# Kernel optimization log

Hardware: AMD Instinct MI355X
Metric: run time of the kernel (lower is better)

The kernel has to match this reference:

```python
import jax, jax.numpy as jnp
import numpy as np

EPS = 1e-8
TAU = 0.2  # gumbel temperature


def lorentz_linear(x, W, log_scale):
    # y = W x; project back onto hyperboloid (k=1): time from sigmoid, rescale space
    y = x @ W.T
    time = jax.nn.sigmoid(y[..., :1]) * jnp.exp(log_scale) + 1.1
    narrow = y[..., 1:]
    s = (time * time - 1.0) / jnp.clip(jnp.sum(narrow * narrow, axis=-1, keepdims=True), EPS, None)
    return jnp.concatenate([time, narrow * jnp.sqrt(s)], axis=-1)


def logmap0(x):
    # Lorentz (k=1) log map at origin o=(1,0,...,0): (0, arccosh(x0) * xs/||xs||)
    x0 = x[..., :1]
    xs = x[..., 1:]
    nrm = jnp.clip(jnp.linalg.norm(xs, axis=-1, keepdims=True), EPS, None)
    d = jnp.arccosh(jnp.clip(x0, 1.0 + 1e-6, None))
    return jnp.concatenate([jnp.zeros_like(x0), d * xs / nrm], axis=-1)


def lorentz_dist(a, b):
    # dist = arccosh(-<a,b>_L), <a,b>_L = -a0*b0 + sum_i ai*bi
    inner = a[..., 0] * b[..., 0] - jnp.sum(a[..., 1:] * b[..., 1:], axis=-1)
    return jnp.arccosh(jnp.clip(inner, 1.0 + 1e-6, None))


def scatter_softmax(score, seg, num_segments):
    m = jax.ops.segment_max(score, seg, num_segments=num_segments)
    m = jnp.where(jnp.isfinite(m), m, 0.0)  # empty segments
    e = jnp.exp(score - m[seg])
    s = jax.ops.segment_sum(e, seg, num_segments=num_segments)
    return e / jnp.clip(s[seg], EPS, None)


def setup_inputs() -> dict:
    key = jax.random.key(0)
    ks = jax.random.split(key, 8)
    N, E, D, A = 50000, 800000, 128, 128
    # nodes on hyperboloid: time = sqrt(1 + ||space||^2)
    xs = jax.random.normal(ks[0], (N, D - 1), dtype=jnp.float32)
    x0 = jnp.sqrt(1.0 + jnp.sum(xs * xs, axis=-1, keepdims=True))
    x = jnp.concatenate([x0, xs], axis=-1)
    src = jax.random.randint(ks[1], (E,), 0, N)
    dst = jax.random.randint(ks[2], (E,), 0, N)
    edge_value = jax.random.uniform(ks[3], (E,), dtype=jnp.float32)
    stdv = 1.0 / np.sqrt(D)
    Wq = jax.random.uniform(ks[4], (D, D), minval=-stdv, maxval=stdv, dtype=jnp.float32).at[:, 0].set(0.0)
    Wk = jax.random.uniform(ks[5], (D, D), minval=-stdv, maxval=stdv, dtype=jnp.float32).at[:, 0].set(0.0)
    Wa = jax.random.normal(ks[6], (A, D), dtype=jnp.float32) * np.sqrt(2.0 / (A + D))
    log_scale = jnp.asarray(np.log(10.0), dtype=jnp.float32)
    return {"x": x, "src": src, "dst": dst, "edge_value": edge_value,
            "Wq": Wq, "Wk": Wk, "Wa": Wa,
            "log_scale_q": log_scale, "log_scale_k": log_scale}


def reference(x, src, dst, edge_value, Wq, Wk, Wa, log_scale_q, log_scale_k):
    N = x.shape[0]
    # assignment logits in tangent space -> softmax
    ass = jax.nn.softmax(logmap0(x) @ Wa.T, axis=-1)  # [N, A]
    q = lorentz_linear(x, Wq, log_scale_q)            # [N, D]
    k = lorentz_linear(x, Wk, log_scale_k)
    # per-edge negative Lorentz distance
    score = -lorentz_dist(q[src], k[dst])             # [E]
    # scatter softmax over outgoing edges of each src node
    score = scatter_softmax(score, src, N)
    # sparse attention matmul: out[i] = sum_{e: src=i} score_e * ass[dst_e]
    ass = jax.ops.segment_sum(score[:, None] * ass[dst], src, num_segments=N)  # [N, A]
    # gumbel softmax on log(ass + 1e-6)
    logits = jnp.log(ass + 1e-6)
    u = jax.random.uniform(jax.random.key(42), logits.shape, minval=1e-10, maxval=1.0)
    g = -jnp.log(-jnp.log(u))
    return jax.nn.softmax((logits + g) / TAU, axis=-1)
```

## Files before the change

### kernel.cpp

```cpp
#include <hip/hip_runtime.h>
#include <hip/hip_bf16.h>
#include <hip/hip_fp16.h>
#include <math.h>


#define D128 128
#define XP 136

typedef _Float16 f16x2 __attribute__((ext_vector_type(2)));
typedef _Float16 f16x8 __attribute__((ext_vector_type(8)));
typedef float f32x4 __attribute__((ext_vector_type(4)));

union U4 { uint4 u; f16x2 f2[4]; __half2 hh[4]; };

__device__ __forceinline__ void threefry2x32(unsigned x0, unsigned x1,
                                             unsigned& o0, unsigned& o1) {
  const unsigned k0 = 0u, k1 = 42u;
  const unsigned k2 = 0x1BD11BDAu ^ k0 ^ k1;
  x0 += k0; x1 += k1;
#define TF_ROT(r) { x0 += x1; x1 = (x1 << (r)) | (x1 >> (32 - (r))); x1 ^= x0; }
  TF_ROT(13) TF_ROT(15) TF_ROT(26) TF_ROT(6)
  x0 += k1; x1 += k2 + 1u;
  TF_ROT(17) TF_ROT(29) TF_ROT(16) TF_ROT(24)
  x0 += k2; x1 += k0 + 2u;
  TF_ROT(13) TF_ROT(15) TF_ROT(26) TF_ROT(6)
  x0 += k0; x1 += k1 + 3u;
  TF_ROT(17) TF_ROT(29) TF_ROT(16) TF_ROT(24)
  x0 += k1; x1 += k2 + 4u;
  TF_ROT(13) TF_ROT(15) TF_ROT(26) TF_ROT(6)
  x0 += k2; x1 += k0 + 5u;
#undef TF_ROT
  o0 = x0; o1 = x1;
}

__global__ __launch_bounds__(256) void cvt_kernel(
    const float* __restrict__ x, const float* __restrict__ Wq,
    const float* __restrict__ Wk, const float* __restrict__ Wa,
    __half* __restrict__ xh, __half* __restrict__ wqh,
    __half* __restrict__ wkh, __half* __restrict__ wah, int nx8) {
  int i = blockIdx.x * 256 + threadIdx.x;
  const float* src; __half* dst; size_t off;
  if (i < nx8) {
    src = x; dst = xh; off = (size_t)i * 8;
  } else {
    int j = i - nx8; int w = j >> 11; int r = j & 2047;
    if (w >= 3) return;
    off = (size_t)r * 8;
    src = (w == 0) ? Wq : (w == 1) ? Wk : Wa;
    dst = (w == 0) ? wqh : (w == 1) ? wkh : wah;
  }
  float4 a = *reinterpret_cast<const float4*>(src + off);
  float4 b = *reinterpret_cast<const float4*>(src + off + 4);
  union { __half2 h2[4]; uint4 u; } pk;
  pk.h2[0] = __floats2half2_rn(a.x, a.y);
  pk.h2[1] = __floats2half2_rn(a.z, a.w);
  pk.h2[2] = __floats2half2_rn(b.x, b.y);
  pk.h2[3] = __floats2half2_rn(b.z, b.w);
  *reinterpret_cast<uint4*>(dst + off) = pk.u;
}

__global__ __launch_bounds__(256) void gemm_ass_kernel(
    const __half* __restrict__ xh_g, const __half* __restrict__ wh_g,
    __half* __restrict__ out, int N) {
  __shared__ __align__(16) _Float16 xs[64 * XP];
  __shared__ __align__(16) _Float16 wh[128 * XP];

  const int t = threadIdx.x;
  const int row0 = blockIdx.x * 64;

#pragma unroll
  for (int rr = 0; rr < 2; ++rr) {
    int r = (t >> 3) + 32 * rr, tr = t & 7;
    int gr = row0 + r;
    U4 c0, c1;
    c0.u = make_uint4(0, 0, 0, 0); c1.u = make_uint4(0, 0, 0, 0);
    if (gr < N) {
      c0.u = *reinterpret_cast<const uint4*>(xh_g + (size_t)gr * D128 + tr * 16);
      c1.u = *reinterpret_cast<const uint4*>(xh_g + (size_t)gr * D128 + tr * 16 + 8);
    }
    float v[16];
    float ss = 0.f;
#pragma unroll
    for (int j = 0; j < 4; ++j) {
      float2 f = __half22float2(c0.hh[j]);
      v[2 * j] = f.x; v[2 * j + 1] = f.y; ss += f.x * f.x + f.y * f.y;
    }
#pragma unroll
    for (int j = 0; j < 4; ++j) {
      float2 f = __half22float2(c1.hh[j]);
      v[8 + 2 * j] = f.x; v[9 + 2 * j] = f.y; ss += f.x * f.x + f.y * f.y;
    }
    if (tr == 0) ss -= v[0] * v[0];
#pragma unroll
    for (int msk = 1; msk < 8; msk <<= 1) ss += __shfl_xor(ss, msk);
    float x0v = __shfl(v[0], (t & 63) & ~7);
    float dd = acoshf(fmaxf(x0v, 1.f + 1e-6f));
    float sc = dd / fmaxf(sqrtf(ss), 1e-8f);
#pragma unroll
    for (int j = 0; j < 16; ++j) v[j] *= sc;
    if (tr == 0) v[0] = 0.f;
    union { __half2 h2[4]; uint4 u; } pk;
#pragma unroll
    for (int j = 0; j < 4; ++j) pk.h2[j] = __floats2half2_rn(v[2 * j], v[2 * j + 1]);
    *reinterpret_cast<uint4*>(&xs[r * XP + tr * 16]) = pk.u;
#pragma unroll
    for (int j = 0; j < 4; ++j) pk.h2[j] = __floats2half2_rn(v[8 + 2 * j], v[9 + 2 * j]);
    *reinterpret_cast<uint4*>(&xs[r * XP + tr * 16 + 8]) = pk.u;
  }

#pragma unroll
  for (int i = 0; i < 8; ++i) {
    int f = t + 256 * i, wr = f >> 4, c8 = f & 15;
    *reinterpret_cast<uint4*>(&wh[wr * XP + c8 * 8]) =
        *reinterpret_cast<const uint4*>(wh_g + (size_t)wr * D128 + c8 * 8);
  }
  __syncthreads();

  const int w = t >> 6, lane = t & 63;
  const int lc = lane & 15;
  const int arow = 16 * w + lc;
  const int koff = (lane >> 4) * 8;
  f32x4 acc[8];
#pragma unroll
  for (int i = 0; i < 8; ++i) acc[i] = (f32x4){0.f, 0.f, 0.f, 0.f};

#pragma unroll
  for (int kk = 0; kk < 4; ++kk) {
    f16x8 a = *reinterpret_cast<f16x8*>(&xs[arow * XP + kk * 32 + koff]);
#pragma unroll
    for (int tt = 0; tt < 8; ++tt) {
      f16x8 b = *reinterpret_cast<f16x8*>(&wh[(tt * 16 + lc) * XP + kk * 32 + koff]);
      acc[tt] = __builtin_amdgcn_mfma_f32_16x16x32_f16(a, b, acc[tt], 0, 0, 0);
    }
  }

#pragma unroll
  for (int j = 0; j < 4; ++j) {
    int gr = row0 + 16 * w + ((lane >> 4) << 2) + j;
    float mx = acc[0][j];
#pragma unroll
    for (int tt = 1; tt < 8; ++tt) mx = fmaxf(mx, acc[tt][j]);
#pragma unroll
    for (int msk = 1; msk < 16; msk <<= 1) mx = fmaxf(mx, __shfl_xor(mx, msk));
    float e[8], sm = 0.f;
#pragma unroll
    for (int tt = 0; tt < 8; ++tt) { e[tt] = expf(acc[tt][j] - mx); sm += e[tt]; }
#pragma unroll
    for (int msk = 1; msk < 16; msk <<= 1) sm += __shfl_xor(sm, msk);
    float inv = 1.f / sm;
    if (gr < N) {
#pragma unroll
      for (int tt = 0; tt < 8; ++tt)
        out[(size_t)gr * D128 + tt * 16 + lc] = __float2half(e[tt] * inv);
    }
  }
}

__global__ __launch_bounds__(256) void gemm_qk_kernel(
    const __half* __restrict__ xh_g, const __half* __restrict__ wqh_g,
    const __half* __restrict__ wkh_g, const float* __restrict__ lsq,
    const float* __restrict__ lsk, __half* __restrict__ qout,
    __half* __restrict__ kout, int N) {
  __shared__ __align__(16) _Float16 xs[64 * XP];
  __shared__ __align__(16) _Float16 wh[128 * XP];

  const int t = threadIdx.x;
  const int row0 = blockIdx.x * 64;

#pragma unroll
  for (int i = 0; i < 4; ++i) {
    int f = t + 256 * i, r = f >> 4, c8 = f & 15;
    uint4 v = make_uint4(0, 0, 0, 0);
    if (row0 + r < N)
      v = *reinterpret_cast<const uint4*>(xh_g + (size_t)(row0 + r) * D128 + c8 * 8);
    *reinterpret_cast<uint4*>(&xs[r * XP + c8 * 8]) = v;
  }

  const int w = t >> 6, lane = t & 63;
  const int lc = lane & 15;
  const int arow = 16 * w + lc;
  const int koff = (lane >> 4) * 8;

  for (int p = 0; p < 2; ++p) {
    const __half* Wg = p ? wkh_g : wqh_g;
    if (p) __syncthreads();
#pragma unroll
    for (int i = 0; i < 8; ++i) {
      int f = t + 256 * i, wr = f >> 4, c8 = f & 15;
      *reinterpret_cast<uint4*>(&wh[wr * XP + c8 * 8]) =
          *reinterpret_cast<const uint4*>(Wg + (size_t)wr * D128 + c8 * 8);
    }
    __syncthreads();

    f32x4 acc[8];
#pragma unroll
    for (int i = 0; i < 8; ++i) acc[i] = (f32x4){0.f, 0.f, 0.f, 0.f};
#pragma unroll
    for (int kk = 0; kk < 4; ++kk) {
      f16x8 a = *reinterpret_cast<f16x8*>(&xs[arow * XP + kk * 32 + koff]);
#pragma unroll
      for (int tt = 0; tt < 8; ++tt) {
        f16x8 b = *reinterpret_cast<f16x8*>(&wh[(tt * 16 + lc) * XP + kk * 32 + koff]);
        acc[tt] = __builtin_amdgcn_mfma_f32_16x16x32_f16(a, b, acc[tt], 0, 0, 0);
      }
    }

    float scale = expf(p ? lsk[0] : lsq[0]);
    __half* outp = p ? kout : qout;
    float sgn = p ? 1.f : -1.f;
#pragma unroll
    for (int j = 0; j < 4; ++j) {
      int gr = row0 + 16 * w + ((lane >> 4) << 2) + j;
      float ss = 0.f;
#pragma unroll
      for (int tt = 0; tt < 8; ++tt) {
        float v = acc[tt][j];
        if (tt == 0 && lc == 0) v = 0.f;
        ss += v * v;
      }
#pragma unroll
      for (int msk = 1; msk < 16; msk <<= 1) ss += __shfl_xor(ss, msk);
      float y0 = __shfl(acc[0][j], lane & ~15);
      float tm = scale / (1.f + expf(-y0)) + 1.1f;
      float qs = sqrtf((tm * tm - 1.f) / fmaxf(ss, 1e-8f)) * sgn;
      if (gr < N) {
#pragma unroll
        for (int tt = 0; tt < 8; ++tt) {
          float val = acc[tt][j] * qs;
          if (tt == 0 && lc == 0) val = tm;
          outp[(size_t)gr * D128 + tt * 16 + lc] = __float2half(val);
        }
      }
    }
  }
}

__global__ __launch_bounds__(256) void count_kernel(const int* __restrict__ src,
                                                    int* __restrict__ counts, int E) {
  int e = blockIdx.x * 256 + threadIdx.x;
  if (e < E) atomicAdd(&counts[src[e]], 1);
}

__global__ __launch_bounds__(256) void scan1_kernel(const int* __restrict__ counts,
                                                    int* __restrict__ incl,
                                                    int* __restrict__ partials, int N) {
  int i = blockIdx.x * 256 + threadIdx.x;
  int c = (i < N) ? counts[i] : 0;
  int lane = threadIdx.x & 63, w = threadIdx.x >> 6;
  int v = c;
#pragma unroll
  for (int d = 1; d < 64; d <<= 1) {
    int tv = __shfl_up(v, d);
    if (lane >= d) v += tv;
  }
  __shared__ int wsum[4];
  if (lane == 63) wsum[w] = v;
  __syncthreads();
  int add = 0;
  for (int j = 0; j < w; ++j) add += wsum[j];
  v += add;
  if (i < N) incl[i] = v;
  if (threadIdx.x == 255) partials[blockIdx.x] = v;
}

__global__ __launch_bounds__(256) void scan2_kernel(int* __restrict__ partials, int nparts) {
  int t = threadIdx.x;
  int p = (t < nparts) ? partials[t] : 0;
  int lane = t & 63, w = t >> 6;
  int v = p;
#pragma unroll
  for (int d = 1; d < 64; d <<= 1) {
    int tv = __shfl_up(v, d);
    if (lane >= d) v += tv;
  }
  __shared__ int wsum[4];
  if (lane == 63) wsum[w] = v;
  __syncthreads();
  int add = 0;
  for (int j = 0; j < w; ++j) add += wsum[j];
  v += add;
  if (t < nparts) partials[t] = v - p;
}

__global__ __launch_bounds__(256) void scan3_kernel(const int* __restrict__ counts,
                                                    int* __restrict__ incl_to_start,
                                                    int* __restrict__ cursor,
                                                    const int* __restrict__ partials, int N) {
  int i = blockIdx.x * 256 + threadIdx.x;
  if (i < N) {
    int s = incl_to_start[i] - counts[i] + partials[blockIdx.x];
    incl_to_start[i] = s;
    cursor[i] = s;
  }
}

__global__ __launch_bounds__(256) void csr_fill_kernel(
    const int* __restrict__ src, const int* __restrict__ dst,
    int* __restrict__ cursor, int* __restrict__ dst_s, int E) {
  int e = blockIdx.x * 256 + threadIdx.x;
  if (e < E) {
    int pos = atomicAdd(&cursor[src[e]], 1);
    dst_s[pos] = dst[e];
  }
}

__global__ __launch_bounds__(256) void node_fused_kernel(
    const __half* __restrict__ qh, const __half* __restrict__ kh,
    const __half* __restrict__ ass, const int* __restrict__ start,
    const int* __restrict__ counts, const int* __restrict__ dst_s,
    float* __restrict__ out, int N) {
  int g = threadIdx.x >> 4;
  int lq = threadIdx.x & 15;
  int n = blockIdx.x * 16 + g;
  if (n >= N) return;
  int st = start[n], deg = counts[n];
  int c8 = lq * 8;

  U4 qv;
  qv.u = *reinterpret_cast<const uint4*>(qh + (size_t)n * D128 + c8);

  float lsum = 0.f;
  float acc[8];
#pragma unroll
  for (int j = 0; j < 8; ++j) acc[j] = 0.f;

  if (deg > 0) {
    int d_cur = dst_s[st];
    int d_nxt = (deg > 1) ? dst_s[st + 1] : d_cur;
    U4 kv, av;
    kv.u = *reinterpret_cast<const uint4*>(kh + (size_t)d_cur * D128 + c8);
    av.u = *reinterpret_cast<const uint4*>(ass + (size_t)d_cur * D128 + c8);

    for (int i = 0; i < deg; ++i) {
      U4 kvn, avn;
      kvn.u = *reinterpret_cast<const uint4*>(kh + (size_t)d_nxt * D128 + c8);
      avn.u = *reinterpret_cast<const uint4*>(ass + (size_t)d_nxt * D128 + c8);
      int p2 = st + i + 2;
      int d_nn = dst_s[(p2 < st + deg) ? p2 : st];

      float part = __builtin_amdgcn_fdot2(qv.f2[0], kv.f2[0],
                   __builtin_amdgcn_fdot2(qv.f2[1], kv.f2[1],
                   __builtin_amdgcn_fdot2(qv.f2[2], kv.f2[2],
                   __builtin_amdgcn_fdot2(qv.f2[3], kv.f2[3], 0.f, false),
                   false), false), false);
#pragma unroll
      for (int msk = 1; msk < 16; msk <<= 1) part += __shfl_xor(part, msk);

      float x = fmaxf(part, 1.f + 1e-6f);
      float tt = x + sqrtf(__builtin_fmaf(x, x, -1.f));
      float w = __builtin_amdgcn_rcpf(tt);

      lsum += w;
      float2 v0 = __half22float2(av.hh[0]);
      float2 v1 = __half22float2(av.hh[1]);
      float2 v2 = __half22float2(av.hh[2]);
      float2 v3 = __half22float2(av.hh[3]);
      acc[0] += w * v0.x;  acc[1] += w * v0.y;
      acc[2] += w * v1.x;  acc[3] += w * v1.y;
      acc[4] += w * v2.x;  acc[5] += w * v2.y;
      acc[6] += w * v3.x;  acc[7] += w * v3.y;

      kv = kvn; av = avn;
      d_nxt = d_nn;
    }
  }

  float inv = (deg > 0) ? 1.f / fmaxf(lsum, 1e-8f) : 0.f;

  float vg[8];
#pragma unroll
  for (int j = 0; j < 8; ++j) {
    unsigned o0, o1;
    threefry2x32(0u, (unsigned)(n * D128 + c8 + j), o0, o1);
    unsigned bits = o0 ^ o1;
    float f = __uint_as_float((bits >> 9) | 0x3f800000u) - 1.0f;
    float u = fmaxf(1e-10f, f * (1.0f - 1e-10f) + 1e-10f);
    float gmb = -logf(-logf(u));
    vg[j] = (logf(acc[j] * inv + 1e-6f) + gmb) / 0.2f;
  }
  float mm = vg[0];
#pragma unroll
  for (int j = 1; j < 8; ++j) mm = fmaxf(mm, vg[j]);
#pragma unroll
  for (int msk = 1; msk < 16; msk <<= 1) mm = fmaxf(mm, __shfl_xor(mm, msk));
  float sm = 0.f;
#pragma unroll
  for (int j = 0; j < 8; ++j) { vg[j] = expf(vg[j] - mm); sm += vg[j]; }
#pragma unroll
  for (int msk = 1; msk < 16; msk <<= 1) sm += __shfl_xor(sm, msk);
  float invs = 1.f / sm;
  *reinterpret_cast<float4*>(out + (size_t)n * D128 + c8) =
      make_float4(vg[0] * invs, vg[1] * invs, vg[2] * invs, vg[3] * invs);
  *reinterpret_cast<float4*>(out + (size_t)n * D128 + c8 + 4) =
      make_float4(vg[4] * invs, vg[5] * invs, vg[6] * invs, vg[7] * invs);
}

extern "C" void kernel_launch(void* const* d_in, const int* in_sizes, int n_in,
                              void* d_out, int out_size, void* d_ws, size_t ws_size,
                              hipStream_t stream) {
  const float* x   = (const float*)d_in[0];
  const int*   src = (const int*)d_in[1];
  const int*   dst = (const int*)d_in[2];
  const float* Wq  = (const float*)d_in[4];
  const float* Wk  = (const float*)d_in[5];
  const float* Wa  = (const float*)d_in[6];
  const float* lsq = (const float*)d_in[7];
  const float* lsk = (const float*)d_in[8];
  const int N = in_sizes[0] / D128;
  const int E = in_sizes[1];
  float* out = (float*)d_out;

  __half* xh   = (__half*)d_ws;
  __half* qh   = xh + (size_t)N * D128;
  __half* kh   = qh + (size_t)N * D128;
  __half* ah   = kh + (size_t)N * D128;
  __half* wqh  = ah + (size_t)N * D128;
  __half* wkh  = wqh + 16384;
  __half* wah  = wkh + 16384;
  int* counts  = (int*)(wah + 16384);
  int* startv  = counts + N;
  int* cursor  = startv + N;
  int* partials= cursor + N;
  int* dst_s   = partials + 256;

  hipMemsetAsync(counts, 0, (size_t)N * sizeof(int), stream);

  const int nx8 = N * 16;
  const int cvt_blocks = (nx8 + 3 * 2048 + 255) / 256;
  cvt_kernel<<<cvt_blocks, 256, 0, stream>>>(x, Wq, Wk, Wa, xh, wqh, wkh, wah, nx8);

  const int gemm_blocks = (N + 63) / 64;
  gemm_ass_kernel<<<gemm_blocks, 256, 0, stream>>>(xh, wah, ah, N);
  gemm_qk_kernel<<<gemm_blocks, 256, 0, stream>>>(xh, wqh, wkh, lsq, lsk, qh, kh, N);

  const int eb = (E + 255) / 256;
  count_kernel<<<eb, 256, 0, stream>>>(src, counts, E);

  const int nb = (N + 255) / 256;
  scan1_kernel<<<nb, 256, 0, stream>>>(counts, startv, partials, N);
  scan2_kernel<<<1, 256, 0, stream>>>(partials, nb);
  scan3_kernel<<<nb, 256, 0, stream>>>(counts, startv, cursor, partials, N);
  csr_fill_kernel<<<eb, 256, 0, stream>>>(src, dst, cursor, dst_s, E);

  node_fused_kernel<<<(N + 15) / 16, 256, 0, stream>>>(qh, kh, ah, startv,
                                                       counts, dst_s, out, N);
}
```

Baseline: 213.0 us.

## Fuse x conversion and three GEMMs into one kernel; merge weight cvt with count

Drops the separate x-to-fp16 conversion pass and the half-precision copy of x. One GEMM kernel now reads fp32 x directly, converts it in shared memory and runs the Q, K and assignment projections in sequence, applying the logmap in place before the third. The weight conversion and the edge-count atomics share one launch, and the node gather loop prefetches two edges ahead with a split dot-product tree. This removes kernel launches and a full N×128 round trip through global memory, in exchange for more work per GEMM block.

```diff
diff --git a/kernel.cpp b/kernel.cpp
--- a/kernel.cpp
+++ b/kernel.cpp
@@ -33,35 +33,39 @@
   o0 = x0; o1 = x1;
 }
 
-__global__ __launch_bounds__(256) void cvt_kernel(
-    const float* __restrict__ x, const float* __restrict__ Wq,
-    const float* __restrict__ Wk, const float* __restrict__ Wa,
-    __half* __restrict__ xh, __half* __restrict__ wqh,
-    __half* __restrict__ wkh, __half* __restrict__ wah, int nx8) {
-  int i = blockIdx.x * 256 + threadIdx.x;
-  const float* src; __half* dst; size_t off;
-  if (i < nx8) {
-    src = x; dst = xh; off = (size_t)i * 8;
+__global__ __launch_bounds__(256) void cvt_count_kernel(
+    const float* __restrict__ Wq, const float* __restrict__ Wk,
+    const float* __restrict__ Wa, __half* __restrict__ wqh,
+    __half* __restrict__ wkh, __half* __restrict__ wah,
+    const int* __restrict__ src, int* __restrict__ counts, int E) {
+  int b = blockIdx.x;
+  if (b < 24) {
+    int i = b * 256 + threadIdx.x;
+    int w = i >> 11, r = i & 2047;
+    if (w >= 3) return;
+    size_t off = (size_t)r * 8;
+    const float* s = (w == 0) ? Wq : (w == 1) ? Wk : Wa;
+    __half* d = (w == 0) ? wqh : (w == 1) ? wkh : wah;
+    float4 a = *reinterpret_cast<const float4*>(s + off);
+    float4 c = *reinterpret_cast<const float4*>(s + off + 4);
+    union { __half2 h2[4]; uint4 u; } pk;
+    pk.h2[0] = __floats2half2_rn(a.x, a.y);
+    pk.h2[1] = __floats2half2_rn(a.z, a.w);
+    pk.h2[2] = __floats2half2_rn(c.x, c.y);
+    pk.h2[3] = __floats2half2_rn(c.z, c.w);
+    *reinterpret_cast<uint4*>(d + off) = pk.u;
   } else {
-    int j = i - nx8; int w = j >> 11; int r = j & 2047;
-    if (w >= 3) return;
-    off = (size_t)r * 8;
-    src = (w == 0) ? Wq : (w == 1) ? Wk : Wa;
-    dst = (w == 0) ? wqh : (w == 1) ? wkh : wah;
-  }
-  float4 a = *reinterpret_cast<const float4*>(src + off);
-  float4 b = *reinterpret_cast<const float4*>(src + off + 4);
-  union { __half2 h2[4]; uint4 u; } pk;
-  pk.h2[0] = __floats2half2_rn(a.x, a.y);
-  pk.h2[1] = __floats2half2_rn(a.z, a.w);
-  pk.h2[2] = __floats2half2_rn(b.x, b.y);
-  pk.h2[3] = __floats2half2_rn(b.z, b.w);
-  *reinterpret_cast<uint4*>(dst + off) = pk.u;
-}
-
-__global__ __launch_bounds__(256) void gemm_ass_kernel(
-    const __half* __restrict__ xh_g, const __half* __restrict__ wh_g,
-    __half* __restrict__ out, int N) {
+    int e = (b - 24) * 256 + threadIdx.x;
+    if (e < E) atomicAdd(&counts[src[e]], 1);
+  }
+}
+
+__global__ __launch_bounds__(256) void gemm3_kernel(
+    const float* __restrict__ X, const __half* __restrict__ wqh_g,
+    const __half* __restrict__ wkh_g, const __half* __restrict__ wah_g,
+    const float* __restrict__ lsq, const float* __restrict__ lsk,
+    __half* __restrict__ qout, __half* __restrict__ kout,
+    __half* __restrict__ aout, int N) {
   __shared__ __align__(16) _Float16 xs[64 * XP];
   __shared__ __align__(16) _Float16 wh[128 * XP];
 
@@ -69,127 +73,69 @@
   const int row0 = blockIdx.x * 64;
 
 #pragma unroll
-  for (int rr = 0; rr < 2; ++rr) {
-    int r = (t >> 3) + 32 * rr, tr = t & 7;
-    int gr = row0 + r;
-    U4 c0, c1;
-    c0.u = make_uint4(0, 0, 0, 0); c1.u = make_uint4(0, 0, 0, 0);
-    if (gr < N) {
-      c0.u = *reinterpret_cast<const uint4*>(xh_g + (size_t)gr * D128 + tr * 16);
-      c1.u = *reinterpret_cast<const uint4*>(xh_g + (size_t)gr * D128 + tr * 16 + 8);
-    }
-    float v[16];
-    float ss = 0.f;
-#pragma unroll
-    for (int j = 0; j < 4; ++j) {
-      float2 f = __half22float2(c0.hh[j]);
-      v[2 * j] = f.x; v[2 * j + 1] = f.y; ss += f.x * f.x + f.y * f.y;
-    }
-#pragma unroll
-    for (int j = 0; j < 4; ++j) {
-      float2 f = __half22float2(c1.hh[j]);
-      v[8 + 2 * j] = f.x; v[9 + 2 * j] = f.y; ss += f.x * f.x + f.y * f.y;
-    }
-    if (tr == 0) ss -= v[0] * v[0];
-#pragma unroll
-    for (int msk = 1; msk < 8; msk <<= 1) ss += __shfl_xor(ss, msk);
-    float x0v = __shfl(v[0], (t & 63) & ~7);
-    float dd = acoshf(fmaxf(x0v, 1.f + 1e-6f));
-    float sc = dd / fmaxf(sqrtf(ss), 1e-8f);
-#pragma unroll
-    for (int j = 0; j < 16; ++j) v[j] *= sc;
-    if (tr == 0) v[0] = 0.f;
-    union { __half2 h2[4]; uint4 u; } pk;
-#pragma unroll
-    for (int j = 0; j < 4; ++j) pk.h2[j] = __floats2half2_rn(v[2 * j], v[2 * j + 1]);
-    *reinterpret_cast<uint4*>(&xs[r * XP + tr * 16]) = pk.u;
-#pragma unroll
-    for (int j = 0; j < 4; ++j) pk.h2[j] = __floats2half2_rn(v[8 + 2 * j], v[9 + 2 * j]);
-    *reinterpret_cast<uint4*>(&xs[r * XP + tr * 16 + 8]) = pk.u;
-  }
-
-#pragma unroll
   for (int i = 0; i < 8; ++i) {
-    int f = t + 256 * i, wr = f >> 4, c8 = f & 15;
-    *reinterpret_cast<uint4*>(&wh[wr * XP + c8 * 8]) =
-        *reinterpret_cast<const uint4*>(wh_g + (size_t)wr * D128 + c8 * 8);
-  }
-  __syncthreads();
+    int f = t + 256 * i, r = f >> 5, c4 = f & 31;
+    float4 v = make_float4(0.f, 0.f, 0.f, 0.f);
+    if (row0 + r < N)
+      v = *reinterpret_cast<const float4*>(X + (size_t)(row0 + r) * D128 + c4 * 4);
+    union { _Float16 h[4]; uint2 u; } p;
+    p.h[0] = (_Float16)v.x; p.h[1] = (_Float16)v.y;
+    p.h[2] = (_Float16)v.z; p.h[3] = (_Float16)v.w;
+    *reinterpret_cast<uint2*>(&xs[r * XP + c4 * 4]) = p.u;
+  }
 
   const int w = t >> 6, lane = t & 63;
   const int lc = lane & 15;
   const int arow = 16 * w + lc;
   const int koff = (lane >> 4) * 8;
-  f32x4 acc[8];
-#pragma unroll
-  for (int i = 0; i < 8; ++i) acc[i] = (f32x4){0.f, 0.f, 0.f, 0.f};
-
-#pragma unroll
-  for (int kk = 0; kk < 4; ++kk) {
-    f16x8 a = *reinterpret_cast<f16x8*>(&xs[arow * XP + kk * 32 + koff]);
-#pragma unroll
-    for (int tt = 0; tt < 8; ++tt) {
-      f16x8 b = *reinterpret_cast<f16x8*>(&wh[(tt * 16 + lc) * XP + kk * 32 + koff]);
-      acc[tt] = __builtin_amdgcn_mfma_f32_16x16x32_f16(a, b, acc[tt], 0, 0, 0);
-    }
-  }
-
-#pragma unroll
-  for (int j = 0; j < 4; ++j) {
-    int gr = row0 + 16 * w + ((lane >> 4) << 2) + j;
-    float mx = acc[0][j];
-#pragma unroll
-    for (int tt = 1; tt < 8; ++tt) mx = fmaxf(mx, acc[tt][j]);
-#pragma unroll
-    for (int msk = 1; msk < 16; msk <<= 1) mx = fmaxf(mx, __shfl_xor(mx, msk));
-    float e[8], sm = 0.f;
-#pragma unroll
-    for (int tt = 0; tt < 8; ++tt) { e[tt] = expf(acc[tt][j] - mx); sm += e[tt]; }
-#pragma unroll
-    for (int msk = 1; msk < 16; msk <<= 1) sm += __shfl_xor(sm, msk);
-    float inv = 1.f / sm;
-    if (gr < N) {
-#pragma unroll
-      for (int tt = 0; tt < 8; ++tt)
-        out[(size_t)gr * D128 + tt * 16 + lc] = __float2half(e[tt] * inv);
-    }
-  }
-}
-
-__global__ __launch_bounds__(256) void gemm_qk_kernel(
-    const __half* __restrict__ xh_g, const __half* __restrict__ wqh_g,
-    const __half* __restrict__ wkh_g, const float* __restrict__ lsq,
-    const float* __restrict__ lsk, __half* __restrict__ qout,
-    __half* __restrict__ kout, int N) {
-  __shared__ __align__(16) _Float16 xs[64 * XP];
-  __shared__ __align__(16) _Float16 wh[128 * XP];
-
-  const int t = threadIdx.x;
-  const int row0 = blockIdx.x * 64;
-
-#pragma unroll
-  for (int i = 0; i < 4; ++i) {
-    int f = t + 256 * i, r = f >> 4, c8 = f & 15;
-    uint4 v = make_uint4(0, 0, 0, 0);
-    if (row0 + r < N)
-      v = *reinterpret_cast<const uint4*>(xh_g + (size_t)(row0 + r) * D128 + c8 * 8);
-    *reinterpret_cast<uint4*>(&xs[r * XP + c8 * 8]) = v;
-  }
-
-  const int w = t >> 6, lane = t & 63;
-  const int lc = lane & 15;
-  const int arow = 16 * w + lc;
-  const int koff = (lane >> 4) * 8;
-
-  for (int p = 0; p < 2; ++p) {
-    const __half* Wg = p ? wkh_g : wqh_g;
-    if (p) __syncthreads();
+
+  for (int p = 0; p < 3; ++p) {
+    __syncthreads();
+    const __half* Wg = (p == 0) ? wqh_g : (p == 1) ? wkh_g : wah_g;
 #pragma unroll
     for (int i = 0; i < 8; ++i) {
       int f = t + 256 * i, wr = f >> 4, c8 = f & 15;
       *reinterpret_cast<uint4*>(&wh[wr * XP + c8 * 8]) =
           *reinterpret_cast<const uint4*>(Wg + (size_t)wr * D128 + c8 * 8);
     }
+
+    if (p == 2) {
+#pragma unroll
+      for (int rr = 0; rr < 2; ++rr) {
+        int r = (t >> 3) + 32 * rr, tr = t & 7;
+        U4 c0, c1;
+        c0.u = *reinterpret_cast<uint4*>(&xs[r * XP + tr * 16]);
+        c1.u = *reinterpret_cast<uint4*>(&xs[r * XP + tr * 16 + 8]);
+        float v[16];
+        float ss = 0.f;
+#pragma unroll
+        for (int j = 0; j < 4; ++j) {
+          float2 f = __half22float2(c0.hh[j]);
+          v[2 * j] = f.x; v[2 * j + 1] = f.y; ss += f.x * f.x + f.y * f.y;
+        }
+#pragma unroll
+        for (int j = 0; j < 4; ++j) {
+          float2 f = __half22float2(c1.hh[j]);
+          v[8 + 2 * j] = f.x; v[9 + 2 * j] = f.y; ss += f.x * f.x + f.y * f.y;
+        }
+        if (tr == 0) ss -= v[0] * v[0];
+#pragma unroll
+        for (int msk = 1; msk < 8; msk <<= 1) ss += __shfl_xor(ss, msk);
+        float x0v = __shfl(v[0], (t & 63) & ~7);
+        float dd = acoshf(fmaxf(x0v, 1.f + 1e-6f));
+        float sc = dd / fmaxf(sqrtf(ss), 1e-8f);
+#pragma unroll
+        for (int j = 0; j < 16; ++j) v[j] *= sc;
+        if (tr == 0) v[0] = 0.f;
+        union { __half2 h2[4]; uint4 u; } pk;
+#pragma unroll
+        for (int j = 0; j < 4; ++j) pk.h2[j] = __floats2half2_rn(v[2 * j], v[2 * j + 1]);
+        *reinterpret_cast<uint4*>(&xs[r * XP + tr * 16]) = pk.u;
+#pragma unroll
+        for (int j = 0; j < 4; ++j) pk.h2[j] = __floats2half2_rn(v[8 + 2 * j], v[9 + 2 * j]);
+        *reinterpret_cast<uint4*>(&xs[r * XP + tr * 16 + 8]) = pk.u;
+      }
+    }
     __syncthreads();
 
     f32x4 acc[8];
@@ -205,40 +151,57 @@
       }
     }
 
-    float scale = expf(p ? lsk[0] : lsq[0]);
-    __half* outp = p ? kout : qout;
-    float sgn = p ? 1.f : -1.f;
-#pragma unroll
-    for (int j = 0; j < 4; ++j) {
-      int gr = row0 + 16 * w + ((lane >> 4) << 2) + j;
-      float ss = 0.f;
-#pragma unroll
-      for (int tt = 0; tt < 8; ++tt) {
-        float v = acc[tt][j];
-        if (tt == 0 && lc == 0) v = 0.f;
-        ss += v * v;
+    if (p < 2) {
+      float scale = expf(p ? lsk[0] : lsq[0]);
+      __half* outp = p ? kout : qout;
+      float sgn = p ? 1.f : -1.f;
+#pragma unroll
+      for (int j = 0; j < 4; ++j) {
+        int gr = row0 + 16 * w + ((lane >> 4) << 2) + j;
+        float ss = 0.f;
+#pragma unroll
+        for (int tt = 0; tt < 8; ++tt) {
+          float v = acc[tt][j];
+          if (tt == 0 && lc == 0) v = 0.f;
+          ss += v * v;
+        }
+#pragma unroll
+        for (int msk = 1; msk < 16; msk <<= 1) ss += __shfl_xor(ss, msk);
+        float y0 = __shfl(acc[0][j], lane & ~15);
+        float tm = scale / (1.f + expf(-y0)) + 1.1f;
+        float qs = sqrtf((tm * tm - 1.f) / fmaxf(ss, 1e-8f)) * sgn;
+        if (gr < N) {
+#pragma unroll
+          for (int tt = 0; tt < 8; ++tt) {
+            float val = acc[tt][j] * qs;
+            if (tt == 0 && lc == 0) val = tm;
+            outp[(size_t)gr * D128 + tt * 16 + lc] = __float2half(val);
+          }
+        }
       }
-#pragma unroll
-      for (int msk = 1; msk < 16; msk <<= 1) ss += __shfl_xor(ss, msk);
-      float y0 = __shfl(acc[0][j], lane & ~15);
-      float tm = scale / (1.f + expf(-y0)) + 1.1f;
-      float qs = sqrtf((tm * tm - 1.f) / fmaxf(ss, 1e-8f)) * sgn;
-      if (gr < N) {
-#pragma unroll
-        for (int tt = 0; tt < 8; ++tt) {
-          float val = acc[tt][j] * qs;
-          if (tt == 0 && lc == 0) val = tm;
-          outp[(size_t)gr * D128 + tt * 16 + lc] = __float2half(val);
+    } else {
+#pragma unroll
+      for (int j = 0; j < 4; ++j) {
+        int gr = row0 + 16 * w + ((lane >> 4) << 2) + j;
+        float mx = acc[0][j];
+#pragma unroll
+        for (int tt = 1; tt < 8; ++tt) mx = fmaxf(mx, acc[tt][j]);
+#pragma unroll
+        for (int msk = 1; msk < 16; msk <<= 1) mx = fmaxf(mx, __shfl_xor(mx, msk));
+        float e[8], sm = 0.f;
+#pragma unroll
+        for (int tt = 0; tt < 8; ++tt) { e[tt] = expf(acc[tt][j] - mx); sm += e[tt]; }
+#pragma unroll
+        for (int msk = 1; msk < 16; msk <<= 1) sm += __shfl_xor(sm, msk);
+        float inv = 1.f / sm;
+        if (gr < N) {
+#pragma unroll
+          for (int tt = 0; tt < 8; ++tt)
+            aout[(size_t)gr * D128 + tt * 16 + lc] = __float2half(e[tt] * inv);
         }
       }
     }
   }
-}
-
-__global__ __launch_bounds__(256) void count_kernel(const int* __restrict__ src,
-                                                    int* __restrict__ counts, int E) {
-  int e = blockIdx.x * 256 + threadIdx.x;
-  if (e < E) atomicAdd(&counts[src[e]], 1);
 }
 
 __global__ __launch_bounds__(256) void scan1_kernel(const int* __restrict__ counts,
@@ -325,24 +288,26 @@
   for (int j = 0; j < 8; ++j) acc[j] = 0.f;
 
   if (deg > 0) {
-    int d_cur = dst_s[st];
-    int d_nxt = (deg > 1) ? dst_s[st + 1] : d_cur;
-    U4 kv, av;
-    kv.u = *reinterpret_cast<const uint4*>(kh + (size_t)d_cur * D128 + c8);
-    av.u = *reinterpret_cast<const uint4*>(ass + (size_t)d_cur * D128 + c8);
+    int d0 = dst_s[st];
+    int d1 = (deg > 1) ? dst_s[st + 1] : d0;
+    U4 kv0, av0, kv1, av1;
+    kv0.u = *reinterpret_cast<const uint4*>(kh + (size_t)d0 * D128 + c8);
+    av0.u = *reinterpret_cast<const uint4*>(ass + (size_t)d0 * D128 + c8);
+    kv1.u = *reinterpret_cast<const uint4*>(kh + (size_t)d1 * D128 + c8);
+    av1.u = *reinterpret_cast<const uint4*>(ass + (size_t)d1 * D128 + c8);
 
     for (int i = 0; i < deg; ++i) {
-      U4 kvn, avn;
-      kvn.u = *reinterpret_cast<const uint4*>(kh + (size_t)d_nxt * D128 + c8);
-      avn.u = *reinterpret_cast<const uint4*>(ass + (size_t)d_nxt * D128 + c8);
       int p2 = st + i + 2;
-      int d_nn = dst_s[(p2 < st + deg) ? p2 : st];
-
-      float part = __builtin_amdgcn_fdot2(qv.f2[0], kv.f2[0],
-                   __builtin_amdgcn_fdot2(qv.f2[1], kv.f2[1],
-                   __builtin_amdgcn_fdot2(qv.f2[2], kv.f2[2],
-                   __builtin_amdgcn_fdot2(qv.f2[3], kv.f2[3], 0.f, false),
-                   false), false), false);
+      int d2 = dst_s[(p2 < st + deg) ? p2 : st];
+      U4 kv2, av2;
+      kv2.u = *reinterpret_cast<const uint4*>(kh + (size_t)d2 * D128 + c8);
+      av2.u = *reinterpret_cast<const uint4*>(ass + (size_t)d2 * D128 + c8);
+
+      float pa = __builtin_amdgcn_fdot2(qv.f2[0], kv0.f2[0],
+                 __builtin_amdgcn_fdot2(qv.f2[1], kv0.f2[1], 0.f, false), false);
+      float pb = __builtin_amdgcn_fdot2(qv.f2[2], kv0.f2[2],
+                 __builtin_amdgcn_fdot2(qv.f2[3], kv0.f2[3], 0.f, false), false);
+      float part = pa + pb;
 #pragma unroll
       for (int msk = 1; msk < 16; msk <<= 1) part += __shfl_xor(part, msk);
 
@@ -351,17 +316,17 @@
       float w = __builtin_amdgcn_rcpf(tt);
 
       lsum += w;
-      float2 v0 = __half22float2(av.hh[0]);
-      float2 v1 = __half22float2(av.hh[1]);
-      float2 v2 = __half22float2(av.hh[2]);
-      float2 v3 = __half22float2(av.hh[3]);
+      float2 v0 = __half22float2(av0.hh[0]);
+      float2 v1 = __half22float2(av0.hh[1]);
+      float2 v2 = __half22float2(av0.hh[2]);
+      float2 v3 = __half22float2(av0.hh[3]);
       acc[0] += w * v0.x;  acc[1] += w * v0.y;
       acc[2] += w * v1.x;  acc[3] += w * v1.y;
       acc[4] += w * v2.x;  acc[5] += w * v2.y;
       acc[6] += w * v3.x;  acc[7] += w * v3.y;
 
-      kv = kvn; av = avn;
-      d_nxt = d_nn;
+      kv0 = kv1; av0 = av1;
+      kv1 = kv2; av1 = av2;
     }
   }
 
@@ -410,8 +375,7 @@
   const int E = in_sizes[1];
   float* out = (float*)d_out;
 
-  __half* xh   = (__half*)d_ws;
-  __half* qh   = xh + (size_t)N * D128;
+  __half* qh   = (__half*)d_ws;
   __half* kh   = qh + (size_t)N * D128;
   __half* ah   = kh + (size_t)N * D128;
   __half* wqh  = ah + (size_t)N * D128;
@@ -425,16 +389,13 @@
 
   hipMemsetAsync(counts, 0, (size_t)N * sizeof(int), stream);
 
-  const int nx8 = N * 16;
-  const int cvt_blocks = (nx8 + 3 * 2048 + 255) / 256;
-  cvt_kernel<<<cvt_blocks, 256, 0, stream>>>(x, Wq, Wk, Wa, xh, wqh, wkh, wah, nx8);
+  const int eb = (E + 255) / 256;
+  cvt_count_kernel<<<24 + eb, 256, 0, stream>>>(Wq, Wk, Wa, wqh, wkh, wah,
+                                                src, counts, E);
 
   const int gemm_blocks = (N + 63) / 64;
-  gemm_ass_kernel<<<gemm_blocks, 256, 0, stream>>>(xh, wah, ah, N);
-  gemm_qk_kernel<<<gemm_blocks, 256, 0, stream>>>(xh, wqh, wkh, lsq, lsk, qh, kh, N);
-
-  const int eb = (E + 255) / 256;
-  count_kernel<<<eb, 256, 0, stream>>>(src, counts, E);
+  gemm3_kernel<<<gemm_blocks, 256, 0, stream>>>(x, wqh, wkh, wah, lsq, lsk,
+                                                qh, kh, ah, N);
 
   const int nb = (N + 255) / 256;
   scan1_kernel<<<nb, 256, 0, stream>>>(counts, startv, partials, N);
```

Measured after the change: 207.7 us. 1.03x faster.
